# Kernel tuning notes

Hardware: AMD Instinct MI355X
Metric: run time of the kernel (lower is better)

Reference implementation:

```python
import jax, jax.numpy as jnp
import numpy as np

N_NODES = 100000
N_EDGES = 3200000
IN_DIM, HID, OUT = 512, 256, 64


def setup_inputs() -> dict:
    key = jax.random.key(0)
    k1, k2, k3, k4, k5, k6 = jax.random.split(key, 6)
    x = jax.random.normal(k1, (N_NODES, IN_DIM), dtype=jnp.float32)
    edge_src = jax.random.randint(k2, (N_EDGES,), 0, N_NODES, dtype=jnp.int32)
    edge_dst = jax.random.randint(k3, (N_EDGES,), 0, N_NODES, dtype=jnp.int32)
    edge_val = jax.random.uniform(k4, (N_EDGES,), dtype=jnp.float32)
    # glorot init as in the original `glorot([input_dim, output_dim])`
    w1 = jax.random.normal(k5, (IN_DIM, HID), dtype=jnp.float32) * np.sqrt(2.0 / (IN_DIM + HID))
    w2 = jax.random.normal(k6, (HID, OUT), dtype=jnp.float32) * np.sqrt(2.0 / (HID + OUT))
    return {"x": x, "edge_src": edge_src, "edge_dst": edge_dst,
            "edge_val": edge_val, "w1": w1, "w2": w2}


def _spmm(edge_src, edge_dst, edge_val, dense):
    # support @ dense : out[i] = sum_j A[i,j] * dense[j], A given as COO edges
    msgs = edge_val[:, None] * dense[edge_dst]            # [E, D] gather
    return jax.ops.segment_sum(msgs, edge_src, num_segments=N_NODES)  # scatter-add


def reference(x, edge_src, edge_dst, edge_val, w1, w2):
    # Layer 1: pre_sup = X @ W1 ; support = A @ pre_sup ; relu (no bias)
    h = jax.nn.relu(_spmm(edge_src, edge_dst, edge_val, x @ w1))  # [N, HID]
    # Layer 2: identity activation
    logits = _spmm(edge_src, edge_dst, edge_val, h @ w2)          # [N, OUT]
    return logits
```

## Files before the change

kernel.cpp:

```cpp
#include <hip/hip_runtime.h>

#define NN 100000
#define NE 3200000
#define IN_DIM 512
#define HID 256
#define OUTD 64
#define NB 196
#define CAP 20480
#define EPB 3125

typedef _Float16 f16x8 __attribute__((ext_vector_type(8)));
typedef _Float16 f16x2 __attribute__((ext_vector_type(2)));
typedef float f32x4 __attribute__((ext_vector_type(4)));

__device__ __forceinline__ void async_copy16(void* lds, const void* g) {
    __builtin_amdgcn_global_load_lds(
        (const __attribute__((address_space(1))) void*)g,
        (__attribute__((address_space(3))) void*)lds, 16, 0, 0);
}

__device__ __forceinline__ void dq4(int w, float m, float* a) {
    int lo = (w & 0x00ff00ff) | 0x64006400;
    int hi = ((w >> 8) & 0x00ff00ff) | 0x64006400;
    f16x2 hl_ = __builtin_bit_cast(f16x2, lo);
    f16x2 hh_ = __builtin_bit_cast(f16x2, hi);
    a[0] = fmaf((float)hl_[0], m, a[0]);
    a[1] = fmaf((float)hh_[0], m, a[1]);
    a[2] = fmaf((float)hl_[1], m, a[2]);
    a[3] = fmaf((float)hh_[1], m, a[3]);
}


__global__ void init_cursor_kernel(int* __restrict__ cursor) {
    int t = threadIdx.x;
    if (t < NB) cursor[t] = t * CAP;
}

__global__ __launch_bounds__(256) void bin_kernel(const int* __restrict__ src,
                                                  const int* __restrict__ dst,
                                                  const float* __restrict__ val,
                                                  int* __restrict__ cursor,
                                                  int2* __restrict__ pairs_tmp,
                                                  int E) {
    __shared__ int s_src[EPB];
    __shared__ int s_dst[EPB];
    __shared__ int s_val[EPB];
    __shared__ int hist[NB];
    __shared__ int base[NB];
    const int t = threadIdx.x;
    const int lo = blockIdx.x * EPB;
    const int cnt = min(E - lo, EPB);
    for (int i = t; i < NB; i += 256) hist[i] = 0;
    for (int i = t; i < cnt; i += 256) {
        s_src[i] = src[lo + i];
        s_dst[i] = dst[lo + i];
        s_val[i] = __float_as_int(val[lo + i]);
    }
    __syncthreads();
    for (int i = t; i < cnt; i += 256) atomicAdd(&hist[s_src[i] >> 9], 1);
    __syncthreads();
    for (int i = t; i < NB; i += 256) {
        base[i] = atomicAdd(&cursor[i], hist[i]);
        hist[i] = 0;
    }
    __syncthreads();
    for (int i = t; i < cnt; i += 256) {
        int s = s_src[i];
        int b = s >> 9;
        int l = atomicAdd(&hist[b], 1);
        int pos = base[b] + l;
        pairs_tmp[pos] = make_int2(s_dst[i] | ((s & 511) << 20), s_val[i]);
    }
}

__global__ void bucket_scan_kernel(const int* __restrict__ cursor,
                                   int* __restrict__ bbase, int* __restrict__ offs) {
    __shared__ int sz[NB];
    int t = threadIdx.x;
    if (t < NB) sz[t] = cursor[t] - t * CAP;
    __syncthreads();
    if (t == 0) {
        int acc = 0;
        for (int i = 0; i < NB; ++i) { bbase[i] = acc; acc += sz[i]; }
        bbase[NB] = acc;
        offs[NN] = acc;
    }
}

#define CSR_LDS 18432
__global__ __launch_bounds__(1024) void csr_kernel(const int* __restrict__ cursor,
                                                   const int* __restrict__ bbase,
                                                   const int2* __restrict__ pairs_tmp,
                                                   const float* __restrict__ scales,
                                                   int* __restrict__ offs,
                                                   int2* __restrict__ pairs) {
    __shared__ int sx[CSR_LDS];
    __shared__ int sv[CSR_LDS];
    __shared__ int cnt[512];
    __shared__ int wsum[8];
    const int b = blockIdx.x;
    const int t = threadIdx.x;
    const int s0 = b << 9;
    const int base = bbase[b];
    const int n_b = cursor[b] - b * CAP;
    const int tlo = b * CAP;
    if (t < 512) cnt[t] = 0;
    __syncthreads();
    for (int i = t; i < n_b; i += 1024) {
        int2 pv = pairs_tmp[tlo + i];
        sx[i] = pv.x;
        sv[i] = pv.y;
        atomicAdd(&cnt[((unsigned)pv.x) >> 20], 1);
    }
    __syncthreads();
    int my = 0, incl = 0;
    if (t < 512) {
        my = cnt[t];
        incl = my;
        #pragma unroll
        for (int d = 1; d < 64; d <<= 1) {
            int y = __shfl_up(incl, d);
            if ((t & 63) >= d) incl += y;
        }
        if ((t & 63) == 63) wsum[t >> 6] = incl;
    }
    __syncthreads();
    if (t == 0) {
        int acc = 0;
        #pragma unroll
        for (int i = 0; i < 8; ++i) { int v = wsum[i]; wsum[i] = acc; acc += v; }
    }
    __syncthreads();
    if (t < 512) {
        int excl = base + incl - my + wsum[t >> 6];
        int s = s0 + t;
        if (s < NN) offs[s] = excl;
        cnt[t] = excl;
    }
    __syncthreads();
    for (int i = t; i < n_b; i += 1024) {
        int x = sx[i];
        int so = ((unsigned)x) >> 20;
        int p = atomicAdd(&cnt[so], 1);
        int dst = x & 0xFFFFF;
        float v = __int_as_float(sv[i]) * scales[dst];
        pairs[p] = make_int2(dst, __float_as_int(v));
    }
}


__global__ void transpose_cast2(const float* __restrict__ w1, const float* __restrict__ w2,
                                _Float16* __restrict__ w1t, _Float16* __restrict__ w2t) {
    int idx = blockIdx.x * blockDim.x + threadIdx.x;
    if (idx < IN_DIM * HID) {
        int k = idx / HID, n = idx % HID;
        w1t[(size_t)n * IN_DIM + k] = (_Float16)w1[idx];
    } else if (idx < IN_DIM * HID + HID * OUTD) {
        int j = idx - IN_DIM * HID;
        int k = j / OUTD, n = j % OUTD;
        w2t[(size_t)n * HID + k] = (_Float16)w2[j];
    }
}


__global__ __launch_bounds__(256) void gemm1_f32a(const float* __restrict__ A,
                                                  const _Float16* __restrict__ Bt,
                                                  unsigned char* __restrict__ qC,
                                                  float* __restrict__ scales,
                                                  int M) {
    __shared__ float    As[128 * 32];
    __shared__ _Float16 Bs[256 * 32];
    __shared__ float    rmaxl[2][128];
    const int tid  = threadIdx.x;
    const int lane = tid & 63;
    const int wave = tid >> 6;
    const int wm = wave >> 1, wn = wave & 1;
    const int m0 = blockIdx.x * 128;

    f32x4 acc[4][8];
    #pragma unroll
    for (int i = 0; i < 4; ++i)
        #pragma unroll
        for (int j = 0; j < 8; ++j) acc[i][j] = (f32x4){0.f, 0.f, 0.f, 0.f};

    for (int k0 = 0; k0 < IN_DIM; k0 += 32) {
        #pragma unroll
        for (int it = 0; it < 4; ++it) {
            int i = it * 256 + tid;
            int r = i >> 3;
            int cp = i & 7;
            int cl = cp ^ (r & 7);
            int gr = m0 + r; if (gr >= M) gr = M - 1;
            async_copy16((char*)As + i * 16, A + (size_t)gr * IN_DIM + k0 + cl * 4);
        }
        #pragma unroll
        for (int it = 0; it < 4; ++it) {
            int i = it * 256 + tid;
            int r = i >> 2;
            int cp = i & 3;
            int cl = cp ^ (r & 3);
            async_copy16((char*)Bs + i * 16, Bt + (size_t)r * IN_DIM + k0 + cl * 8);
        }
        __syncthreads();

        const int kc = lane >> 4;
        f16x8 af[4];
        #pragma unroll
        for (int m = 0; m < 4; ++m) {
            int r = wm * 64 + m * 16 + (lane & 15);
            int p0 = (2 * kc) ^ (r & 7);
            int p1 = (2 * kc + 1) ^ (r & 7);
            f32x4 c0 = *(const f32x4*)((const char*)As + r * 128 + p0 * 16);
            f32x4 c1 = *(const f32x4*)((const char*)As + r * 128 + p1 * 16);
            f16x8 v = { (_Float16)c0[0], (_Float16)c0[1], (_Float16)c0[2], (_Float16)c0[3],
                        (_Float16)c1[0], (_Float16)c1[1], (_Float16)c1[2], (_Float16)c1[3] };
            af[m] = v;
        }
        f16x8 bf[8];
        #pragma unroll
        for (int n = 0; n < 8; ++n) {
            int r = wn * 128 + n * 16 + (lane & 15);
            bf[n] = *(const f16x8*)((const char*)Bs + r * 64 + ((kc ^ (r & 3)) * 16));
        }
        #pragma unroll
        for (int m = 0; m < 4; ++m)
            #pragma unroll
            for (int n = 0; n < 8; ++n)
                acc[m][n] = __builtin_amdgcn_mfma_f32_16x16x32_f16(af[m], bf[n], acc[m][n], 0, 0, 0);
        __syncthreads();
    }

    #pragma unroll
    for (int m = 0; m < 4; ++m)
        #pragma unroll
        for (int r = 0; r < 4; ++r) {
            float mm = 0.f;
            #pragma unroll
            for (int n = 0; n < 8; ++n) mm = fmaxf(mm, fabsf(acc[m][n][r]));
            #pragma unroll
            for (int d = 1; d < 16; d <<= 1) mm = fmaxf(mm, __shfl_xor(mm, d));
            if ((lane & 15) == 0)
                rmaxl[wn][wm * 64 + m * 16 + (lane >> 4) * 4 + r] = mm;
        }
    __syncthreads();
    #pragma unroll
    for (int m = 0; m < 4; ++m)
        #pragma unroll
        for (int r = 0; r < 4; ++r) {
            int lrow = wm * 64 + m * 16 + (lane >> 4) * 4 + r;
            int row = m0 + lrow;
            float full = fmaxf(fmaxf(rmaxl[0][lrow], rmaxl[1][lrow]), 1e-12f);
            float inv = 127.0f / full;
            if (row < M) {
                #pragma unroll
                for (int n = 0; n < 8; ++n) {
                    int col = wn * 128 + n * 16 + (lane & 15);
                    qC[(size_t)row * HID + col] =
                        (unsigned char)(__float2int_rn(acc[m][n][r] * inv) + 128);
                }
                if (wn == 0 && (lane & 15) == 0) scales[row] = full * (1.0f / 127.0f);
            }
        }
}


__global__ __launch_bounds__(256) void spmm_relu_mm2(const int* __restrict__ offs,
                                                     const int2* __restrict__ pairs,
                                                     const unsigned char* __restrict__ qpre,
                                                     const float* __restrict__ scales,
                                                     const _Float16* __restrict__ w2t,
                                                     unsigned char* __restrict__ qh2,
                                                     float* __restrict__ ratio2, int n) {
    __shared__ __align__(16) char hl_raw[16 * 528];
    __shared__ float rmax2[4][16];
    const int tid  = threadIdx.x;
    const int lane = tid & 63;
    const int wid  = tid >> 6;
    const int par  = lane >> 4;
    const int fl   = lane & 15;
    const int nbase = blockIdx.x * 16;
    const unsigned char* qbase = qpre + fl * 16;

    #pragma unroll 1
    for (int i = 0; i < 4; ++i) {
        const int node = nbase + wid * 4 + i;
        const int beg = offs[node], end = offs[node + 1];
        float a[16] = {};
        float msum = 0.f;
        int k = beg;
        for (; k + 16 <= end; k += 16) {
            int2 pr[4];
            #pragma unroll
            for (int j = 0; j < 4; ++j) pr[j] = pairs[k + 4 * j + par];
            int4 qv[4];
            #pragma unroll
            for (int j = 0; j < 4; ++j)
                qv[j] = *(const int4*)(qbase + (size_t)pr[j].x * HID);
            #pragma unroll
            for (int j = 0; j < 4; ++j) {
                float m = __int_as_float(pr[j].y);
                msum += m;
                dq4(qv[j].x, m, a + 0);
                dq4(qv[j].y, m, a + 4);
                dq4(qv[j].z, m, a + 8);
                dq4(qv[j].w, m, a + 12);
            }
        }
        if (k < end) {
            int2 pr[4];
            float m_[4];
            #pragma unroll
            for (int j = 0; j < 4; ++j) {
                int idx = k + 4 * j + par;
                int cidx = idx < end ? idx : end - 1;
                pr[j] = pairs[cidx];
                m_[j] = idx < end ? __int_as_float(pr[j].y) : 0.f;
            }
            int4 qv[4];
            #pragma unroll
            for (int j = 0; j < 4; ++j)
                qv[j] = *(const int4*)(qbase + (size_t)pr[j].x * HID);
            #pragma unroll
            for (int j = 0; j < 4; ++j) {
                float m = m_[j];
                msum += m;
                dq4(qv[j].x, m, a + 0);
                dq4(qv[j].y, m, a + 4);
                dq4(qv[j].z, m, a + 8);
                dq4(qv[j].w, m, a + 12);
            }
        }
        #pragma unroll
        for (int q = 0; q < 16; ++q) {
            a[q] += __shfl_xor(a[q], 16);
            a[q] += __shfl_xor(a[q], 32);
        }
        msum += __shfl_xor(msum, 16);
        msum += __shfl_xor(msum, 32);
        if (par == 0) {
            float bias = 1152.f * msum;
            f16x8 o0, o1;
            #pragma unroll
            for (int q = 0; q < 8; ++q) {
                o0[q] = (_Float16)fmaxf(a[q] - bias, 0.f);
                o1[q] = (_Float16)fmaxf(a[8 + q] - bias, 0.f);
            }
            char* bp = hl_raw + (wid * 4 + i) * 528 + fl * 16;
            *(f16x8*)bp         = o0;
            *(f16x8*)(bp + 256) = o1;
        }
    }
    __syncthreads();

    const int r  = lane & 15;
    const int kc = lane >> 4;
    f32x4 acc = (f32x4){0.f, 0.f, 0.f, 0.f};
    #pragma unroll
    for (int kk = 0; kk < 8; ++kk) {
        int c = kk * 4 + kc;
        f16x8 af = *(const f16x8*)(hl_raw + r * 528 + ((c & 1) << 8) + ((c >> 1) << 4));
        f16x8 bf = *(const f16x8*)(w2t + (size_t)(wid * 16 + r) * HID + kk * 32 + kc * 8);
        acc = __builtin_amdgcn_mfma_f32_16x16x32_f16(af, bf, acc, 0, 0, 0);
    }
    float mxv[4];
    #pragma unroll
    for (int j = 0; j < 4; ++j) {
        float mm = fabsf(acc[j]);
        #pragma unroll
        for (int d = 1; d < 16; d <<= 1) mm = fmaxf(mm, __shfl_xor(mm, d));
        mxv[j] = mm;
    }
    if (r == 0) {
        #pragma unroll
        for (int j = 0; j < 4; ++j) rmax2[wid][kc * 4 + j] = mxv[j];
    }
    __syncthreads();
    #pragma unroll
    for (int j = 0; j < 4; ++j) {
        int ln = kc * 4 + j;
        int node = nbase + ln;
        float full = fmaxf(fmaxf(fmaxf(rmax2[0][ln], rmax2[1][ln]),
                                 fmaxf(rmax2[2][ln], rmax2[3][ln])), 1e-12f);
        qh2[(size_t)node * OUTD + wid * 16 + r] =
            (unsigned char)(__float2int_rn(acc[j] * (127.0f / full)) + 128);
        if (wid == 0 && r == 0)
            ratio2[node] = full * (1.0f / 127.0f) / scales[node];
    }
}


__global__ __launch_bounds__(256) void spmm64_q(const int* __restrict__ offs,
                                                const int2* __restrict__ pairs,
                                                const unsigned char* __restrict__ qh2,
                                                const float* __restrict__ ratio2,
                                                float* __restrict__ out, int n) {
    int node = blockIdx.x * 4 + (threadIdx.x >> 6);
    if (node >= n) return;
    int lane = threadIdx.x & 63;
    int par = lane >> 2;
    int fl  = lane & 3;
    int beg = offs[node], end = offs[node + 1];
    const unsigned char* qbase = qh2 + fl * 16;
    float a[16] = {};
    float msum = 0.f;
    int k = beg;
    for (; k + 32 <= end; k += 32) {
        int2 pr[2];
        #pragma unroll
        for (int j = 0; j < 2; ++j) pr[j] = pairs[k + 16 * j + par];
        float rt[2];
        #pragma unroll
        for (int j = 0; j < 2; ++j) rt[j] = ratio2[pr[j].x];
        int4 qv[2];
        #pragma unroll
        for (int j = 0; j < 2; ++j)
            qv[j] = *(const int4*)(qbase + (size_t)pr[j].x * OUTD);
        #pragma unroll
        for (int j = 0; j < 2; ++j) {
            float m = __int_as_float(pr[j].y) * rt[j];
            msum += m;
            dq4(qv[j].x, m, a + 0);
            dq4(qv[j].y, m, a + 4);
            dq4(qv[j].z, m, a + 8);
            dq4(qv[j].w, m, a + 12);
        }
    }
    if (k < end) {
        int2 pr[2];
        float m_[2];
        #pragma unroll
        for (int j = 0; j < 2; ++j) {
            int idx = k + 16 * j + par;
            int cidx = idx < end ? idx : end - 1;
            pr[j] = pairs[cidx];
            m_[j] = idx < end ? __int_as_float(pr[j].y) * ratio2[pr[j].x] : 0.f;
        }
        int4 qv[2];
        #pragma unroll
        for (int j = 0; j < 2; ++j)
            qv[j] = *(const int4*)(qbase + (size_t)pr[j].x * OUTD);
        #pragma unroll
        for (int j = 0; j < 2; ++j) {
            float m = m_[j];
            msum += m;
            dq4(qv[j].x, m, a + 0);
            dq4(qv[j].y, m, a + 4);
            dq4(qv[j].z, m, a + 8);
            dq4(qv[j].w, m, a + 12);
        }
    }
    #pragma unroll
    for (int q = 0; q < 16; ++q) {
        a[q] += __shfl_xor(a[q], 4);
        a[q] += __shfl_xor(a[q], 8);
        a[q] += __shfl_xor(a[q], 16);
        a[q] += __shfl_xor(a[q], 32);
    }
    msum += __shfl_xor(msum, 4);
    msum += __shfl_xor(msum, 8);
    msum += __shfl_xor(msum, 16);
    msum += __shfl_xor(msum, 32);
    if (par == 0) {
        float bias = 1152.f * msum;
        float* ob = out + (size_t)node * OUTD + fl * 16;
        #pragma unroll
        for (int c = 0; c < 4; ++c) {
            float4 o = make_float4(a[4 * c] - bias, a[4 * c + 1] - bias,
                                   a[4 * c + 2] - bias, a[4 * c + 3] - bias);
            *(float4*)(ob + 4 * c) = o;
        }
    }
}


extern "C" void kernel_launch(void* const* d_in, const int* in_sizes, int n_in,
                              void* d_out, int out_size, void* d_ws, size_t ws_size,
                              hipStream_t stream) {
    const float* x    = (const float*)d_in[0];
    const int*   esrc = (const int*)d_in[1];
    const int*   edst = (const int*)d_in[2];
    const float* eval = (const float*)d_in[3];
    const float* w1   = (const float*)d_in[4];
    const float* w2   = (const float*)d_in[5];
    float* out = (float*)d_out;

    char* ws = (char*)d_ws;
    unsigned char* qpre   = (unsigned char*)(ws + 0);
    unsigned char* qh2    = (unsigned char*)(ws + 25600000);
    float*        scales  = (float*)(ws + 32000000);
    float*        ratio2  = (float*)(ws + 32400000);
    int2*         pairs   = (int2*)(ws + 32800000);
    int2*         pairs_t = (int2*)(ws + 58400000);
    int*          cursor  = (int*)(ws + 90512640);
    int*          bbase   = (int*)(ws + 90513664);
    int*          offs    = (int*)(ws + 90514688);
    _Float16*     w1t     = (_Float16*)(ws + 90914816);
    _Float16*     w2t     = (_Float16*)(ws + 91176960);

    init_cursor_kernel<<<1, 256, 0, stream>>>(cursor);
    bin_kernel<<<1024, 256, 0, stream>>>(esrc, edst, eval, cursor, pairs_t, NE);
    bucket_scan_kernel<<<1, 256, 0, stream>>>(cursor, bbase, offs);

    transpose_cast2<<<(IN_DIM * HID + HID * OUTD + 255) / 256, 256, 0, stream>>>(w1, w2, w1t, w2t);
    gemm1_f32a<<<(NN + 127) / 128, 256, 0, stream>>>(x, w1t, qpre, scales, NN);

    csr_kernel<<<NB, 1024, 0, stream>>>(cursor, bbase, pairs_t, scales, offs, pairs);

    spmm_relu_mm2<<<NN / 16, 256, 0, stream>>>(offs, pairs, qpre, scales, w2t, qh2, ratio2, NN);

    spmm64_q<<<(NN + 3) / 4, 256, 0, stream>>>(offs, pairs, qh2, ratio2, out, NN);
}
```

Measured before the change: 426.1 us.

## Merge GEMM1 and edge binning into one launch, fold cursor init into prep

The cursor initialisation is folded into the weight transpose/cast kernel, and the first GEMM and the edge binning pass now run as disjoint block ranges of one kernel sharing a union LDS buffer. This lets the compute-bound GEMM and the memory-bound binning overlap on the GPU and removes two launches. The dequant helper also switches to inline v_fma_mix_f32 assembly so the fp16 conversion and FMA happen in one instruction. The shared LDS size is the larger of the two bodies, which may lower occupancy for the binning blocks, and the binning blocks are scheduled after the GEMM blocks.

```diff
diff --git a/kernel.cpp b/kernel.cpp
--- a/kernel.cpp
+++ b/kernel.cpp
@@ -8,9 +8,10 @@
 #define NB 196
 #define CAP 20480
 #define EPB 3125
+#define GEMM1_BLOCKS 782
+#define MEGA_LDS 39072
 
 typedef _Float16 f16x8 __attribute__((ext_vector_type(8)));
-typedef _Float16 f16x2 __attribute__((ext_vector_type(2)));
 typedef float f32x4 __attribute__((ext_vector_type(4)));
 
 __device__ __forceinline__ void async_copy16(void* lds, const void* g) {
@@ -22,33 +23,142 @@
 __device__ __forceinline__ void dq4(int w, float m, float* a) {
     int lo = (w & 0x00ff00ff) | 0x64006400;
     int hi = ((w >> 8) & 0x00ff00ff) | 0x64006400;
-    f16x2 hl_ = __builtin_bit_cast(f16x2, lo);
-    f16x2 hh_ = __builtin_bit_cast(f16x2, hi);
-    a[0] = fmaf((float)hl_[0], m, a[0]);
-    a[1] = fmaf((float)hh_[0], m, a[1]);
-    a[2] = fmaf((float)hl_[1], m, a[2]);
-    a[3] = fmaf((float)hh_[1], m, a[3]);
-}
-
-
-__global__ void init_cursor_kernel(int* __restrict__ cursor) {
-    int t = threadIdx.x;
-    if (t < NB) cursor[t] = t * CAP;
-}
-
-__global__ __launch_bounds__(256) void bin_kernel(const int* __restrict__ src,
-                                                  const int* __restrict__ dst,
-                                                  const float* __restrict__ val,
-                                                  int* __restrict__ cursor,
-                                                  int2* __restrict__ pairs_tmp,
-                                                  int E) {
-    __shared__ int s_src[EPB];
-    __shared__ int s_dst[EPB];
-    __shared__ int s_val[EPB];
-    __shared__ int hist[NB];
-    __shared__ int base[NB];
+    asm("v_fma_mix_f32 %0, %1, %2, %0 op_sel:[0,0,0] op_sel_hi:[1,0,0]" : "+v"(a[0]) : "v"(lo), "v"(m));
+    asm("v_fma_mix_f32 %0, %1, %2, %0 op_sel:[0,0,0] op_sel_hi:[1,0,0]" : "+v"(a[1]) : "v"(hi), "v"(m));
+    asm("v_fma_mix_f32 %0, %1, %2, %0 op_sel:[1,0,0] op_sel_hi:[1,0,0]" : "+v"(a[2]) : "v"(lo), "v"(m));
+    asm("v_fma_mix_f32 %0, %1, %2, %0 op_sel:[1,0,0] op_sel_hi:[1,0,0]" : "+v"(a[3]) : "v"(hi), "v"(m));
+}
+
+
+__global__ void prep_kernel(const float* __restrict__ w1, const float* __restrict__ w2,
+                            _Float16* __restrict__ w1t, _Float16* __restrict__ w2t,
+                            int* __restrict__ cursor) {
+    int idx = blockIdx.x * blockDim.x + threadIdx.x;
+    if (idx < NB) cursor[idx] = idx * CAP;
+    if (idx < IN_DIM * HID) {
+        int k = idx / HID, n = idx % HID;
+        w1t[(size_t)n * IN_DIM + k] = (_Float16)w1[idx];
+    } else if (idx < IN_DIM * HID + HID * OUTD) {
+        int j = idx - IN_DIM * HID;
+        int k = j / OUTD, n = j % OUTD;
+        w2t[(size_t)n * HID + k] = (_Float16)w2[j];
+    }
+}
+
+
+__device__ __forceinline__ void gemm1_body(char* smem, int bx,
+                                           const float* __restrict__ A,
+                                           const _Float16* __restrict__ Bt,
+                                           unsigned char* __restrict__ qC,
+                                           float* __restrict__ scales, int M) {
+    float*    As    = (float*)smem;
+    _Float16* Bs    = (_Float16*)(smem + 16384);
+    float*    rmaxl = (float*)(smem + 32768);
+    const int tid  = threadIdx.x;
+    const int lane = tid & 63;
+    const int wave = tid >> 6;
+    const int wm = wave >> 1, wn = wave & 1;
+    const int m0 = bx * 128;
+
+    f32x4 acc[4][8];
+    #pragma unroll
+    for (int i = 0; i < 4; ++i)
+        #pragma unroll
+        for (int j = 0; j < 8; ++j) acc[i][j] = (f32x4){0.f, 0.f, 0.f, 0.f};
+
+    for (int k0 = 0; k0 < IN_DIM; k0 += 32) {
+        #pragma unroll
+        for (int it = 0; it < 4; ++it) {
+            int i = it * 256 + tid;
+            int r = i >> 3;
+            int cp = i & 7;
+            int cl = cp ^ (r & 7);
+            int gr = m0 + r; if (gr >= M) gr = M - 1;
+            async_copy16((char*)As + i * 16, A + (size_t)gr * IN_DIM + k0 + cl * 4);
+        }
+        #pragma unroll
+        for (int it = 0; it < 4; ++it) {
+            int i = it * 256 + tid;
+            int r = i >> 2;
+            int cp = i & 3;
+            int cl = cp ^ (r & 3);
+            async_copy16((char*)Bs + i * 16, Bt + (size_t)r * IN_DIM + k0 + cl * 8);
+        }
+        __syncthreads();
+
+        const int kc = lane >> 4;
+        f16x8 af[4];
+        #pragma unroll
+        for (int m = 0; m < 4; ++m) {
+            int r = wm * 64 + m * 16 + (lane & 15);
+            int p0 = (2 * kc) ^ (r & 7);
+            int p1 = (2 * kc + 1) ^ (r & 7);
+            f32x4 c0 = *(const f32x4*)((const char*)As + r * 128 + p0 * 16);
+            f32x4 c1 = *(const f32x4*)((const char*)As + r * 128 + p1 * 16);
+            f16x8 v = { (_Float16)c0[0], (_Float16)c0[1], (_Float16)c0[2], (_Float16)c0[3],
+                        (_Float16)c1[0], (_Float16)c1[1], (_Float16)c1[2], (_Float16)c1[3] };
+            af[m] = v;
+        }
+        f16x8 bf[8];
+        #pragma unroll
+        for (int n = 0; n < 8; ++n) {
+            int r = wn * 128 + n * 16 + (lane & 15);
+            bf[n] = *(const f16x8*)((const char*)Bs + r * 64 + ((kc ^ (r & 3)) * 16));
+        }
+        #pragma unroll
+        for (int m = 0; m < 4; ++m)
+            #pragma unroll
+            for (int n = 0; n < 8; ++n)
+                acc[m][n] = __builtin_amdgcn_mfma_f32_16x16x32_f16(af[m], bf[n], acc[m][n], 0, 0, 0);
+        __syncthreads();
+    }
+
+    #pragma unroll
+    for (int m = 0; m < 4; ++m)
+        #pragma unroll
+        for (int r = 0; r < 4; ++r) {
+            float mm = 0.f;
+            #pragma unroll
+            for (int n = 0; n < 8; ++n) mm = fmaxf(mm, fabsf(acc[m][n][r]));
+            #pragma unroll
+            for (int d = 1; d < 16; d <<= 1) mm = fmaxf(mm, __shfl_xor(mm, d));
+            if ((lane & 15) == 0)
+                rmaxl[wn * 128 + wm * 64 + m * 16 + (lane >> 4) * 4 + r] = mm;
+        }
+    __syncthreads();
+    #pragma unroll
+    for (int m = 0; m < 4; ++m)
+        #pragma unroll
+        for (int r = 0; r < 4; ++r) {
+            int lrow = wm * 64 + m * 16 + (lane >> 4) * 4 + r;
+            int row = m0 + lrow;
+            float full = fmaxf(fmaxf(rmaxl[lrow], rmaxl[128 + lrow]), 1e-12f);
+            float inv = 127.0f / full;
+            if (row < M) {
+                #pragma unroll
+                for (int n = 0; n < 8; ++n) {
+                    int col = wn * 128 + n * 16 + (lane & 15);
+                    qC[(size_t)row * HID + col] =
+                        (unsigned char)(__float2int_rn(acc[m][n][r] * inv) + 128);
+                }
+                if (wn == 0 && (lane & 15) == 0) scales[row] = full * (1.0f / 127.0f);
+            }
+        }
+}
+
+__device__ __forceinline__ void bin_body(char* smem, int bx,
+                                         const int* __restrict__ src,
+                                         const int* __restrict__ dst,
+                                         const float* __restrict__ val,
+                                         int* __restrict__ cursor,
+                                         int2* __restrict__ pairs_tmp, int E) {
+    int* s_src = (int*)smem;
+    int* s_dst = (int*)(smem + 12500);
+    int* s_val = (int*)(smem + 25000);
+    int* hist  = (int*)(smem + 37500);
+    int* base  = (int*)(smem + 38284);
     const int t = threadIdx.x;
-    const int lo = blockIdx.x * EPB;
+    const int lo = bx * EPB;
     const int cnt = min(E - lo, EPB);
     for (int i = t; i < NB; i += 256) hist[i] = 0;
     for (int i = t; i < cnt; i += 256) {
@@ -73,6 +183,23 @@
     }
 }
 
+__global__ __launch_bounds__(256) void mega_kernel(const float* __restrict__ x,
+                                                   const _Float16* __restrict__ w1t,
+                                                   unsigned char* __restrict__ qpre,
+                                                   float* __restrict__ scales,
+                                                   const int* __restrict__ src,
+                                                   const int* __restrict__ dst,
+                                                   const float* __restrict__ val,
+                                                   int* __restrict__ cursor,
+                                                   int2* __restrict__ pairs_tmp) {
+    __shared__ __align__(16) char smem[MEGA_LDS];
+    if (blockIdx.x < GEMM1_BLOCKS)
+        gemm1_body(smem, blockIdx.x, x, w1t, qpre, scales, NN);
+    else
+        bin_body(smem, blockIdx.x - GEMM1_BLOCKS, src, dst, val, cursor, pairs_tmp, NE);
+}
+
+
 __global__ void bucket_scan_kernel(const int* __restrict__ cursor,
                                    int* __restrict__ bbase, int* __restrict__ offs) {
     __shared__ int sz[NB];
@@ -86,6 +213,7 @@
         offs[NN] = acc;
     }
 }
+
 
 #define CSR_LDS 18432
 __global__ __launch_bounds__(1024) void csr_kernel(const int* __restrict__ cursor,
@@ -149,121 +277,6 @@
 }
 
 
-__global__ void transpose_cast2(const float* __restrict__ w1, const float* __restrict__ w2,
-                                _Float16* __restrict__ w1t, _Float16* __restrict__ w2t) {
-    int idx = blockIdx.x * blockDim.x + threadIdx.x;
-    if (idx < IN_DIM * HID) {
-        int k = idx / HID, n = idx % HID;
-        w1t[(size_t)n * IN_DIM + k] = (_Float16)w1[idx];
-    } else if (idx < IN_DIM * HID + HID * OUTD) {
-        int j = idx - IN_DIM * HID;
-        int k = j / OUTD, n = j % OUTD;
-        w2t[(size_t)n * HID + k] = (_Float16)w2[j];
-    }
-}
-
-
-__global__ __launch_bounds__(256) void gemm1_f32a(const float* __restrict__ A,
-                                                  const _Float16* __restrict__ Bt,
-                                                  unsigned char* __restrict__ qC,
-                                                  float* __restrict__ scales,
-                                                  int M) {
-    __shared__ float    As[128 * 32];
-    __shared__ _Float16 Bs[256 * 32];
-    __shared__ float    rmaxl[2][128];
-    const int tid  = threadIdx.x;
-    const int lane = tid & 63;
-    const int wave = tid >> 6;
-    const int wm = wave >> 1, wn = wave & 1;
-    const int m0 = blockIdx.x * 128;
-
-    f32x4 acc[4][8];
-    #pragma unroll
-    for (int i = 0; i < 4; ++i)
-        #pragma unroll
-        for (int j = 0; j < 8; ++j) acc[i][j] = (f32x4){0.f, 0.f, 0.f, 0.f};
-
-    for (int k0 = 0; k0 < IN_DIM; k0 += 32) {
-        #pragma unroll
-        for (int it = 0; it < 4; ++it) {
-            int i = it * 256 + tid;
-            int r = i >> 3;
-            int cp = i & 7;
-            int cl = cp ^ (r & 7);
-            int gr = m0 + r; if (gr >= M) gr = M - 1;
-            async_copy16((char*)As + i * 16, A + (size_t)gr * IN_DIM + k0 + cl * 4);
-        }
-        #pragma unroll
-        for (int it = 0; it < 4; ++it) {
-            int i = it * 256 + tid;
-            int r = i >> 2;
-            int cp = i & 3;
-            int cl = cp ^ (r & 3);
-            async_copy16((char*)Bs + i * 16, Bt + (size_t)r * IN_DIM + k0 + cl * 8);
-        }
-        __syncthreads();
-
-        const int kc = lane >> 4;
-        f16x8 af[4];
-        #pragma unroll
-        for (int m = 0; m < 4; ++m) {
-            int r = wm * 64 + m * 16 + (lane & 15);
-            int p0 = (2 * kc) ^ (r & 7);
-            int p1 = (2 * kc + 1) ^ (r & 7);
-            f32x4 c0 = *(const f32x4*)((const char*)As + r * 128 + p0 * 16);
-            f32x4 c1 = *(const f32x4*)((const char*)As + r * 128 + p1 * 16);
-            f16x8 v = { (_Float16)c0[0], (_Float16)c0[1], (_Float16)c0[2], (_Float16)c0[3],
-                        (_Float16)c1[0], (_Float16)c1[1], (_Float16)c1[2], (_Float16)c1[3] };
-            af[m] = v;
-        }
-        f16x8 bf[8];
-        #pragma unroll
-        for (int n = 0; n < 8; ++n) {
-            int r = wn * 128 + n * 16 + (lane & 15);
-            bf[n] = *(const f16x8*)((const char*)Bs + r * 64 + ((kc ^ (r & 3)) * 16));
-        }
-        #pragma unroll
-        for (int m = 0; m < 4; ++m)
-            #pragma unroll
-            for (int n = 0; n < 8; ++n)
-                acc[m][n] = __builtin_amdgcn_mfma_f32_16x16x32_f16(af[m], bf[n], acc[m][n], 0, 0, 0);
-        __syncthreads();
-    }
-
-    #pragma unroll
-    for (int m = 0; m < 4; ++m)
-        #pragma unroll
-        for (int r = 0; r < 4; ++r) {
-            float mm = 0.f;
-            #pragma unroll
-            for (int n = 0; n < 8; ++n) mm = fmaxf(mm, fabsf(acc[m][n][r]));
-            #pragma unroll
-            for (int d = 1; d < 16; d <<= 1) mm = fmaxf(mm, __shfl_xor(mm, d));
-            if ((lane & 15) == 0)
-                rmaxl[wn][wm * 64 + m * 16 + (lane >> 4) * 4 + r] = mm;
-        }
-    __syncthreads();
-    #pragma unroll
-    for (int m = 0; m < 4; ++m)
-        #pragma unroll
-        for (int r = 0; r < 4; ++r) {
-            int lrow = wm * 64 + m * 16 + (lane >> 4) * 4 + r;
-            int row = m0 + lrow;
-            float full = fmaxf(fmaxf(rmaxl[0][lrow], rmaxl[1][lrow]), 1e-12f);
-            float inv = 127.0f / full;
-            if (row < M) {
-                #pragma unroll
-                for (int n = 0; n < 8; ++n) {
-                    int col = wn * 128 + n * 16 + (lane & 15);
-                    qC[(size_t)row * HID + col] =
-                        (unsigned char)(__float2int_rn(acc[m][n][r] * inv) + 128);
-                }
-                if (wn == 0 && (lane & 15) == 0) scales[row] = full * (1.0f / 127.0f);
-            }
-        }
-}
-
-
 __global__ __launch_bounds__(256) void spmm_relu_mm2(const int* __restrict__ offs,
                                                      const int2* __restrict__ pairs,
                                                      const unsigned char* __restrict__ qpre,
@@ -497,13 +510,13 @@
     _Float16*     w1t     = (_Float16*)(ws + 90914816);
     _Float16*     w2t     = (_Float16*)(ws + 91176960);
 
-    init_cursor_kernel<<<1, 256, 0, stream>>>(cursor);
-    bin_kernel<<<1024, 256, 0, stream>>>(esrc, edst, eval, cursor, pairs_t, NE);
+    prep_kernel<<<(IN_DIM * HID + HID * OUTD + 255) / 256, 256, 0, stream>>>(w1, w2, w1t, w2t, cursor);
+
+    mega_kernel<<<GEMM1_BLOCKS + 1024, 256, 0, stream>>>(x, w1t, qpre, scales,
+                                                         esrc, edst, eval, cursor, pairs_t);
+
     bucket_scan_kernel<<<1, 256, 0, stream>>>(cursor, bbase, offs);
 
-    transpose_cast2<<<(IN_DIM * HID + HID * OUTD + 255) / 256, 256, 0, stream>>>(w1, w2, w1t, w2t);
-    gemm1_f32a<<<(NN + 127) / 128, 256, 0, stream>>>(x, w1t, qpre, scales, NN);
-
     csr_kernel<<<NB, 1024, 0, stream>>>(cursor, bbase, pairs_t, scales, offs, pairs);
 
     spmm_relu_mm2<<<NN / 16, 256, 0, stream>>>(offs, pairs, qpre, scales, w2t, qh2, ratio2, NN);
```

Result: faster. 387.3 us (-9.1%).
